# Performance work log

Hardware: AMD Instinct MI355X
Metric: run time of the kernel (lower is better)

Reference implementation:

```python
import jax, jax.numpy as jnp
import numpy as np

B, S, D, H, HZ = 4096, 64, 9, 128, 32
DT = 0.1


def _lstm_cell(x, h, c, Wih, Whh, bih, bhh):
    gates = x @ Wih.T + bih + h @ Whh.T + bhh
    i, f, g, o = jnp.split(gates, 4, axis=-1)
    c_new = jax.nn.sigmoid(f) * c + jax.nn.sigmoid(i) * jnp.tanh(g)
    h_new = jax.nn.sigmoid(o) * jnp.tanh(c_new)
    return h_new, c_new


def _forward(input_batch, W_ih_enc, W_hh_enc, b_ih_enc, b_hh_enc, W_e, V_e, v_e,
             W_d, V_d, v_d, W_ih_dec, W_hh_dec, b_ih_dec, b_hh_dec,
             W_out, b_out, scaler_mean, scaler_std, pos_mean):
    bsz = input_batch.shape[0]
    # ---- encoder with input attention ----
    x_perm = jnp.swapaxes(input_batch, 1, 2)          # (B, D, S)
    attn_input = jnp.einsum('bds,ts->bdt', x_perm, V_e)  # V_e * x^i, precomputed once
    h0 = jnp.zeros((bsz, H), input_batch.dtype)
    c0 = jnp.zeros((bsz, H), input_batch.dtype)

    def enc_step(carry, x_t):
        h, c = carry
        attn_hidden = jnp.concatenate([h, c], axis=1) @ W_e.T          # (B, S)
        comb = jnp.tanh(attn_hidden[:, None, :] + attn_input)          # (B, D, S)
        e = comb @ v_e                                                 # (B, D)
        alpha = jax.nn.softmax(e, axis=1)
        h, c = _lstm_cell(alpha * x_t, h, c, W_ih_enc, W_hh_enc, b_ih_enc, b_hh_enc)
        return (h, c), h

    (h_enc, c_enc), hs = jax.lax.scan(enc_step, (h0, c0), jnp.swapaxes(input_batch, 0, 1))
    enc_hidden = jnp.swapaxes(hs, 0, 1)               # (B, S, H)
    attn_encoder = enc_hidden @ V_d.T                 # V_d * h_j, precomputed once

    # ---- initial physics state ----
    pos = input_batch[:, -1, :3] + pos_mean
    vel = input_batch[:, -1, 3:6] * scaler_std + scaler_mean
    pre_vel = input_batch[:, -2, 3:6] * scaler_std + scaler_mean
    acc = (vel - pre_vel) / DT

    def dec_step(carry, _):
        d, c, pos, vel, acc = carry
        attn_dec = jnp.concatenate([d, c], axis=1) @ W_d.T             # (B, H)
        comb = jnp.tanh(attn_dec[:, None, :] + attn_encoder)           # (B, S, H)
        beta = jax.nn.softmax(comb @ v_d, axis=1)                      # (B, S)
        context = jnp.einsum('bs,bsh->bh', beta, enc_hidden)           # (B, H)
        phys = jnp.concatenate([pos - pos_mean,
                                (vel - scaler_mean) / scaler_std,
                                acc / scaler_std], axis=1)             # (B, 9)
        d, c = _lstm_cell(jnp.concatenate([phys, context], axis=1), d, c,
                          W_ih_dec, W_hh_dec, b_ih_dec, b_hh_dec)
        pred_acc = (jnp.concatenate([d, context], axis=1) @ W_out.T + b_out) * scaler_std
        pos_pred = pos + vel * DT + 0.5 * acc * DT * DT                # Verlet position
        vel_new = vel + 0.5 * (acc + pred_acc) * DT                    # Verlet velocity
        out = jnp.concatenate([pos_pred, vel_new, pred_acc], axis=1)   # (B, 9)
        return (d, c, pos_pred, vel_new, pred_acc), out

    _, outs = jax.lax.scan(dec_step, (h_enc, c_enc, pos, vel, acc), None, length=HZ)
    return jnp.swapaxes(outs, 0, 1)                   # (B, HZ, 9)


def setup_inputs() -> dict:
    key = jax.random.key(0)
    ks = jax.random.split(key, 16)
    p = lambda k, shape, s=0.05: jax.random.normal(k, shape, dtype=jnp.float32) * s
    return dict(
        input_batch=jax.random.normal(ks[0], (B, S, D), dtype=jnp.float32),
        W_ih_enc=p(ks[1], (4 * H, D)), W_hh_enc=p(ks[2], (4 * H, H)),
        b_ih_enc=jnp.zeros((4 * H,), jnp.float32), b_hh_enc=jnp.zeros((4 * H,), jnp.float32),
        W_e=p(ks[3], (S, 2 * H)), V_e=p(ks[4], (S, S)), v_e=p(ks[5], (S,)),
        W_d=p(ks[6], (H, 2 * H)), V_d=p(ks[7], (H, H)), v_d=p(ks[8], (H,)),
        W_ih_dec=p(ks[9], (4 * H, 9 + H)), W_hh_dec=p(ks[10], (4 * H, H)),
        b_ih_dec=jnp.zeros((4 * H,), jnp.float32), b_hh_dec=jnp.zeros((4 * H,), jnp.float32),
        W_out=p(ks[11], (3, 2 * H)), b_out=jnp.zeros((3,), jnp.float32),
        scaler_mean=p(ks[12], (3,), 0.1),
        scaler_std=jnp.abs(p(ks[13], (3,), 0.1)) + 1.0,
        pos_mean=p(ks[14], (3,), 0.1),
    )


def reference(input_batch, W_ih_enc, W_hh_enc, b_ih_enc, b_hh_enc, W_e, V_e, v_e,
              W_d, V_d, v_d, W_ih_dec, W_hh_dec, b_ih_dec, b_hh_dec,
              W_out, b_out, scaler_mean, scaler_std, pos_mean):
    return _forward(input_batch, W_ih_enc, W_hh_enc, b_ih_enc, b_hh_enc, W_e, V_e, v_e,
                    W_d, V_d, v_d, W_ih_dec, W_hh_dec, b_ih_dec, b_hh_dec,
                    W_out, b_out, scaler_mean, scaler_std, pos_mean)
```

## Files before the change

kernel.cpp:

```cpp
#include <hip/hip_runtime.h>
#include <hip/hip_bf16.h>
#include <hip/hip_fp8.h>

#define B_   4096
#define S_   64
#define D_   9
#define H_   128
#define HZ_  32
#define DT_  0.1f

#define OFF_WET    0
#define OFF_VET    16384
#define OFF_WENCT  20480
#define OFF_BENC   90624
#define OFF_WDT    91136
#define OFF_WDECT  123904
#define OFF_BDEC   259584
#define OFF_WOUTT  260096
#define OFF_VDT    260864
#define OFF_DECD   277248
#define OFF_DECC   801536
#define F32_TOTAL  1325824
#define PREP_N     277248


typedef __bf16 bf16x8 __attribute__((ext_vector_type(8)));
typedef float  f32x4  __attribute__((ext_vector_type(4)));

__device__ __forceinline__ float fast_tanh(float x) {
    float e = __expf(2.0f * x);
    return 1.0f - __fdividef(2.0f, e + 1.0f);
}
__device__ __forceinline__ float sigf(float x) {
    return __fdividef(1.0f, 1.0f + __expf(-x));
}
__device__ __forceinline__ float bf_lo(unsigned int u) { return __uint_as_float(u << 16); }
__device__ __forceinline__ float bf_hi(unsigned int u) { return __uint_as_float(u & 0xffff0000u); }
__device__ __forceinline__ float bfu2f(unsigned short u) { return __uint_as_float((unsigned int)u << 16); }
__device__ __forceinline__ unsigned short f2bfu(float f) {
    __hip_bfloat16 b = __float2bfloat16(f);
    return *(unsigned short*)&b;
}
__device__ __forceinline__ unsigned int pack_bf(float lo, float hi) {
    return (unsigned int)f2bfu(lo) | ((unsigned int)f2bfu(hi) << 16);
}
__device__ __forceinline__ float f8tof(unsigned int byte) {
    __hip_fp8_e4m3 t; t.__x = (unsigned char)byte; return (float)t;
}
__device__ __forceinline__ unsigned char f2f8(float f) {
    __hip_fp8_e4m3 q(f); return q.__x;
}
__device__ __forceinline__ unsigned int pack4_f8(float a, float b, float c, float d) {
    return (unsigned int)f2f8(a) | ((unsigned int)f2f8(b) << 8) |
           ((unsigned int)f2f8(c) << 16) | ((unsigned int)f2f8(d) << 24);
}

__global__ void prep_kernel(const float* __restrict__ Wih_e, const float* __restrict__ Whh_e,
    const float* __restrict__ bih_e, const float* __restrict__ bhh_e,
    const float* __restrict__ W_e, const float* __restrict__ V_e,
    const float* __restrict__ W_d, const float* __restrict__ V_d,
    const float* __restrict__ Wih_d, const float* __restrict__ Whh_d,
    const float* __restrict__ bih_d, const float* __restrict__ bhh_d,
    const float* __restrict__ W_out, float* __restrict__ ws) {
  for (int idx = blockIdx.x * blockDim.x + threadIdx.x; idx < PREP_N;
       idx += gridDim.x * blockDim.x) {
    int i = idx;
    if (i < 16384) { continue; }
    i -= 16384;
    if (i < 4096) { int s = i >> 6, t = i & 63; ws[OFF_VET + i] = V_e[t * 64 + s]; continue; }
    i -= 4096;
    if (i < 70144) { continue; }
    i -= 70144;
    if (i < 512) { ws[OFF_BENC + i] = bih_e[i] + bhh_e[i]; continue; }
    i -= 512;
    if (i < 32768) { continue; }
    i -= 32768;
    if (i < 135680) { continue; }
    i -= 135680;
    if (i < 512) { ws[OFF_BDEC + i] = bih_d[i] + bhh_d[i]; continue; }
    i -= 512;
    if (i < 768) { int k = i / 3, j = i % 3; ws[OFF_WOUTT + i] = W_out[j * 256 + k]; continue; }
  }
}

__global__ void prep_mfma_kernel(const float* __restrict__ W_d,
    const float* __restrict__ Wih_d, const float* __restrict__ Whh_d,
    unsigned short* __restrict__ WdTm, unsigned short* __restrict__ WdecTm) {
  int idx = blockIdx.x * blockDim.x + threadIdx.x;
  if (idx < 32768) {
    int j = idx & 7, l = (idx >> 3) & 63, t = idx >> 9;
    int nt = t & 7, ks = t >> 3;
    int k = ks * 32 + (l >> 4) * 8 + j;
    int n = nt * 16 + (l & 15);
    WdTm[idx] = f2bfu(W_d[n * 256 + k]);
    return;
  }
  int i2 = idx - 32768;
  if (i2 < 147456) {
    int j = i2 & 7, l = (i2 >> 3) & 63, t = i2 >> 9;
    int ks = t % 9, tile = t / 9;
    int q = tile & 3, is = tile >> 2;
    int k = ks * 32 + (l >> 4) * 8 + j;
    int g = q * 128 + is * 16 + (l & 15);
    float v;
    if (k < 128)      v = Whh_d[g * 128 + k];
    else if (k < 256) v = Wih_d[g * 137 + 9 + (k - 128)];
    else if (k < 265) v = Wih_d[g * 137 + (k - 256)];
    else              v = 0.f;
    WdecTm[i2] = f2bfu(v);
  }
}

__global__ void prep_enc_mfma_kernel(const float* __restrict__ W_e,
    const float* __restrict__ Wih_e, const float* __restrict__ Whh_e,
    const float* __restrict__ V_d,
    unsigned short* __restrict__ WeTm, unsigned short* __restrict__ WencTm,
    unsigned short* __restrict__ VdTm) {
  int idx = blockIdx.x * blockDim.x + threadIdx.x;
  if (idx < 16384) {
    int j = idx & 7, l = (idx >> 3) & 63, tile = idx >> 9;
    int nt = tile & 3, ks = tile >> 2;
    int k = ks * 32 + (l >> 4) * 8 + j;
    int n = nt * 16 + (l & 15);
    WeTm[idx] = f2bfu(W_e[n * 256 + k]);
    return;
  }
  int i2 = idx - 16384;
  if (i2 < 81920) {
    int j = i2 & 7, l = (i2 >> 3) & 63, tile = i2 >> 9;
    int ks = tile % 5, tq = tile / 5;
    int q = tq & 3, is = tq >> 2;
    int kk = (l >> 4) * 8 + j;
    int g = q * 128 + is * 16 + (l & 15);
    float v;
    if (ks < 4) v = Whh_e[g * 128 + ks * 32 + kk];
    else        v = (kk < 9) ? Wih_e[g * 9 + kk] : 0.f;
    WencTm[i2] = f2bfu(v);
    return;
  }
  int i3 = i2 - 81920;
  if (i3 < 16384) {
    int j = i3 & 7, l = (i3 >> 3) & 63, tile = i3 >> 9;
    int nt = tile & 7, ks = tile >> 3;
    int i = ks * 32 + (l >> 4) * 8 + j;
    int n = nt * 16 + (l & 15);
    VdTm[i3] = f2bfu(V_d[n * 128 + i]);
  }
}

__global__ __launch_bounds__(512, 1) void encoder_mfma_kernel(
    const float* __restrict__ x_in, const float* __restrict__ ws,
    const float* __restrict__ v_e_g,
    const unsigned short* __restrict__ WeTm, const unsigned short* __restrict__ WencTm,
    __hip_bfloat16* __restrict__ EH,
    unsigned short* __restrict__ dG, float* __restrict__ cG) {
  __shared__ unsigned short hA[2][16 * 296];
  __shared__ float cF[16 * 132];
  __shared__ float ahL[16 * 64];
  __shared__ unsigned short aiL[16 * 576];
  __shared__ unsigned short xbL[16 * 576];

  const int tid = threadIdx.x;
  const int b0 = blockIdx.x * 16;
  const int l = tid & 63, w = tid >> 6;
  const int quad = l >> 4, l15 = l & 15;

  for (int i = tid; i < 16 * 576; i += 512) {
    int m = i / 576, r = i % 576;
    xbL[i] = f2bfu(x_in[(size_t)(b0 + m) * 576 + r]);
  }
  for (int i = tid; i < 2 * 16 * 296; i += 512) ((unsigned short*)hA)[i] = 0;
  for (int i = tid; i < 16 * 132; i += 512) cF[i] = 0.f;
  __syncthreads();

  {
    const float* __restrict__ VeT = ws + OFF_VET;
    for (int i = tid; i < 16 * 576; i += 512) {
      int t = i & 63, dd = (i >> 6) % 9, m = i / 576;
      float acc = 0.f;
      for (int s = 0; s < 64; ++s) acc += bfu2f(xbL[m * 576 + s * 9 + dd]) * VeT[s * 64 + t];
      aiL[m * 576 + dd * 64 + t] = f2bfu(acc);
    }
  }
  const float ve_r = v_e_g[l];
  const int ig = w * 16 + l15;
  float bbq[4];
  #pragma unroll
  for (int q = 0; q < 4; ++q) bbq[q] = ws[OFF_BENC + q * 128 + ig];
  __syncthreads();

  for (int t = 0; t < S_; ++t) {
    unsigned short* bufC = hA[t & 1];
    unsigned short* bufN = hA[(t + 1) & 1];
    if (w < 4) {
      f32x4 acc = {0.f, 0.f, 0.f, 0.f};
      #pragma unroll
      for (int ks = 0; ks < 8; ++ks) {
        uint4 au = *(const uint4*)&bufC[l15 * 296 + ks * 32 + quad * 8];
        uint4 bu = *(const uint4*)(WeTm + (size_t)((ks * 4 + w) * 64 + l) * 8);
        acc = __builtin_amdgcn_mfma_f32_16x16x32_bf16(
            __builtin_bit_cast(bf16x8, au), __builtin_bit_cast(bf16x8, bu), acc, 0, 0, 0);
      }
      #pragma unroll
      for (int r = 0; r < 4; ++r)
        ahL[(quad * 4 + r) * 64 + w * 16 + l15] = acc[r];
    }
    __syncthreads();
    {
      const int m0 = 2 * w, m1 = 2 * w + 1;
      float a0 = ahL[m0 * 64 + l], a1 = ahL[m1 * 64 + l];
      float e0k = -1e30f, e1k = -1e30f;
      #pragma unroll
      for (int dd = 0; dd < 9; ++dd) {
        float t0 = fast_tanh(a0 + bfu2f(aiL[m0 * 576 + dd * 64 + l])) * ve_r;
        float t1 = fast_tanh(a1 + bfu2f(aiL[m1 * 576 + dd * 64 + l])) * ve_r;
        #pragma unroll
        for (int off = 32; off; off >>= 1) {
          t0 += __shfl_xor(t0, off, 64);
          t1 += __shfl_xor(t1, off, 64);
        }
        if (l == dd) { e0k = t0; e1k = t1; }
      }
      float mx0 = e0k, mx1 = e1k;
      #pragma unroll
      for (int off = 8; off; off >>= 1) {
        mx0 = fmaxf(mx0, __shfl_xor(mx0, off, 64));
        mx1 = fmaxf(mx1, __shfl_xor(mx1, off, 64));
      }
      float ex0 = (l < 9) ? __expf(e0k - mx0) : 0.f;
      float ex1 = (l < 9) ? __expf(e1k - mx1) : 0.f;
      float s0 = ex0, s1 = ex1;
      #pragma unroll
      for (int off = 8; off; off >>= 1) {
        s0 += __shfl_xor(s0, off, 64);
        s1 += __shfl_xor(s1, off, 64);
      }
      if (l < 9) {
        bufC[m0 * 296 + 256 + l] = f2bfu(__fdividef(ex0, s0) * bfu2f(xbL[m0 * 576 + t * 9 + l]));
        bufC[m1 * 296 + 256 + l] = f2bfu(__fdividef(ex1, s1) * bfu2f(xbL[m1 * 576 + t * 9 + l]));
      }
    }
    __syncthreads();
    {
      uint4 af[5];
      #pragma unroll
      for (int ks = 0; ks < 4; ++ks)
        af[ks] = *(const uint4*)&bufC[l15 * 296 + ks * 32 + quad * 8];
      af[4] = *(const uint4*)&bufC[l15 * 296 + 256 + quad * 8];
      f32x4 g4[4];
      #pragma unroll
      for (int q = 0; q < 4; ++q) {
        f32x4 acc = {0.f, 0.f, 0.f, 0.f};
        #pragma unroll
        for (int ks = 0; ks < 5; ++ks) {
          uint4 bu = *(const uint4*)(WencTm + (size_t)(((w * 4 + q) * 5 + ks) * 64 + l) * 8);
          acc = __builtin_amdgcn_mfma_f32_16x16x32_bf16(
              __builtin_bit_cast(bf16x8, af[ks]), __builtin_bit_cast(bf16x8, bu), acc, 0, 0, 0);
        }
        g4[q] = acc;
      }
      #pragma unroll
      for (int r = 0; r < 4; ++r) {
        int m = quad * 4 + r;
        float gi = g4[0][r] + bbq[0];
        float gf = g4[1][r] + bbq[1];
        float gg = g4[2][r] + bbq[2];
        float go = g4[3][r] + bbq[3];
        float co = cF[m * 132 + ig];
        float cn = sigf(gf) * co + sigf(gi) * fast_tanh(gg);
        float hn = sigf(go) * fast_tanh(cn);
        cF[m * 132 + ig] = cn;
        bufN[m * 296 + ig] = f2bfu(hn);
        bufN[m * 296 + 128 + ig] = f2bfu(cn);
        EH[((size_t)(b0 + m) * S_ + t) * H_ + ig] = __float2bfloat16(hn);
      }
    }
    __syncthreads();
  }
  for (int i = tid; i < 16 * 128; i += 512) {
    int m = i >> 7, ii = i & 127;
    dG[(size_t)(b0 + m) * 128 + ii] = hA[0][m * 296 + ii];
    cG[(size_t)(b0 + m) * 128 + ii] = cF[m * 132 + ii];
  }
}

__global__ __launch_bounds__(256) void attnenc_mfma_kernel(
    const unsigned short* __restrict__ EH, const unsigned short* __restrict__ VdTm,
    unsigned char* __restrict__ AETf8, unsigned char* __restrict__ EHf8) {
  const int tid = threadIdx.x;
  const int b = blockIdx.x * 4 + (tid >> 6);
  const int l = tid & 63;
  const int quad = l >> 4, l15 = l & 15;

  const unsigned short* ehb = EH + (size_t)b * 8192;
  uint4 A[4][4];
  #pragma unroll
  for (int st = 0; st < 4; ++st)
    #pragma unroll
    for (int ks = 0; ks < 4; ++ks)
      A[st][ks] = *(const uint4*)(ehb + (st * 16 + l15) * 128 + ks * 32 + quad * 8);

  {
    unsigned char* e8b = EHf8 + (size_t)b * 8192;
    #pragma unroll
    for (int st = 0; st < 4; ++st)
      #pragma unroll
      for (int ks = 0; ks < 4; ++ks) {
        uint4 a = A[st][ks];
        uint2 pk;
        pk.x = pack4_f8(bf_lo(a.x), bf_hi(a.x), bf_lo(a.y), bf_hi(a.y));
        pk.y = pack4_f8(bf_lo(a.z), bf_hi(a.z), bf_lo(a.w), bf_hi(a.w));
        *(uint2*)(e8b + (st * 16 + l15) * 128 + ks * 32 + quad * 8) = pk;
      }
  }

  unsigned char* outb = AETf8 + (size_t)b * 8192;
  const int k = l15;
  #pragma unroll
  for (int nt = 0; nt < 8; ++nt) {
    uint4 Bf[4];
    #pragma unroll
    for (int ks = 0; ks < 4; ++ks)
      Bf[ks] = *(const uint4*)(VdTm + (size_t)((ks * 8 + nt) * 64 + l) * 8);
    int kg = nt * 16 + k;
    int kb = kg >> 3, k7 = kg & 7;
    #pragma unroll
    for (int st = 0; st < 4; ++st) {
      f32x4 acc = {0.f, 0.f, 0.f, 0.f};
      #pragma unroll
      for (int ks = 0; ks < 4; ++ks)
        acc = __builtin_amdgcn_mfma_f32_16x16x32_bf16(
            __builtin_bit_cast(bf16x8, A[st][ks]), __builtin_bit_cast(bf16x8, Bf[ks]), acc, 0, 0, 0);
      #pragma unroll
      for (int r = 0; r < 4; ++r) {
        int s = st * 16 + quad * 4 + r;
        outb[kb * 512 + s * 8 + k7] = f2f8(acc[r]);
      }
    }
  }
}

__global__ __launch_bounds__(256) void init_dec_kernel(
    const float* __restrict__ x_in,
    const unsigned short* __restrict__ dG, const float* __restrict__ cG,
    const unsigned short* __restrict__ WdTm,
    const float* __restrict__ smean_g, const float* __restrict__ sstd_g,
    const float* __restrict__ pmean_g,
    unsigned short* __restrict__ adG, float* __restrict__ pvsG) {
  __shared__ unsigned short dcB[16 * 264];
  const int tid = threadIdx.x;
  const int b0 = blockIdx.x * 16;
  const int l = tid & 63, w = tid >> 6;
  const int quad = l >> 4, l15 = l & 15;

  {
    int m = tid >> 4, i0 = (tid & 15) * 8;
    *(uint4*)&dcB[m * 264 + i0] = *(const uint4*)(dG + (size_t)(b0 + m) * 128 + i0);
    float4 c0 = *(const float4*)(cG + (size_t)(b0 + m) * 128 + i0);
    float4 c1 = *(const float4*)(cG + (size_t)(b0 + m) * 128 + i0 + 4);
    uint4 pk;
    pk.x = pack_bf(c0.x, c0.y); pk.y = pack_bf(c0.z, c0.w);
    pk.z = pack_bf(c1.x, c1.y); pk.w = pack_bf(c1.z, c1.w);
    *(uint4*)&dcB[m * 264 + 128 + i0] = pk;
  }
  if (tid < 48) {
    int m = tid / 3, jj = tid % 3;
    const float* xi = x_in + (size_t)(b0 + m) * 576;
    float sm = smean_g[jj], ss = sstd_g[jj], pm = pmean_g[jj];
    float v  = xi[63 * 9 + 3 + jj] * ss + sm;
    float pv = xi[62 * 9 + 3 + jj] * ss + sm;
    float* P = pvsG + (size_t)(b0 + m) * 12;
    P[jj] = xi[63 * 9 + jj] + pm;
    P[3 + jj] = v;
    P[6 + jj] = (v - pv) / DT_;
  }
  __syncthreads();
  #pragma unroll
  for (int t = 0; t < 2; ++t) {
    const int nt = w + 4 * t;
    f32x4 acc = {0.f, 0.f, 0.f, 0.f};
    #pragma unroll
    for (int ks = 0; ks < 8; ++ks) {
      uint4 au = *(const uint4*)&dcB[l15 * 264 + ks * 32 + quad * 8];
      uint4 bu = *(const uint4*)(WdTm + (size_t)((ks * 8 + nt) * 64 + l) * 8);
      acc = __builtin_amdgcn_mfma_f32_16x16x32_bf16(
          __builtin_bit_cast(bf16x8, au), __builtin_bit_cast(bf16x8, bu), acc, 0, 0, 0);
    }
    int n = nt * 16 + l15;
    #pragma unroll
    for (int r = 0; r < 4; ++r)
      adG[(size_t)(b0 + quad * 4 + r) * 128 + n] = f2bfu(acc[r]);
  }
}

__global__ __launch_bounds__(256, 8) void attn_step_kernel(
    const unsigned char* __restrict__ AETf8, const unsigned char* __restrict__ EHf8,
    const unsigned short* __restrict__ adG, const float* __restrict__ v_d_g,
    unsigned short* __restrict__ ctxG) {
  __shared__ unsigned short adL[2 * 128];
  __shared__ float vdL[128];
  __shared__ float scp[2][2][64];
  __shared__ float bet[2][64];
  __shared__ float ctxP[2][2][128];

  const int tid = threadIdx.x;
  const int b0 = blockIdx.x * 2;
  const int l = tid & 63, w = tid >> 6;
  const int ml = w >> 1, half = w & 1;
  const int quad = l >> 4, l15 = l & 15;

  if (tid < 32)
    *(uint4*)&adL[tid * 8] = *(const uint4*)(adG + (size_t)(b0 + (tid >> 4)) * 128 + (tid & 15) * 8);
  if (tid < 128) vdL[tid] = v_d_g[tid];
  __syncthreads();

  {
    const unsigned char* aet = AETf8 + (size_t)(b0 + ml) * 8192 + (size_t)half * 8 * 512;
    const unsigned short* adp = adL + ml * 128 + half * 64;
    float e = 0.f;
    #pragma unroll
    for (int kb = 0; kb < 8; ++kb) {
      uint2 av = *(const uint2*)(aet + kb * 512 + l * 8);
      uint4 ad8 = *(const uint4*)(adp + kb * 8);
      float4 v0 = *(const float4*)&vdL[half * 64 + kb * 8];
      float4 v1 = *(const float4*)&vdL[half * 64 + kb * 8 + 4];
      e += fast_tanh(bf_lo(ad8.x) + f8tof(av.x))       * v0.x;
      e += fast_tanh(bf_hi(ad8.x) + f8tof(av.x >> 8))  * v0.y;
      e += fast_tanh(bf_lo(ad8.y) + f8tof(av.x >> 16)) * v0.z;
      e += fast_tanh(bf_hi(ad8.y) + f8tof(av.x >> 24)) * v0.w;
      e += fast_tanh(bf_lo(ad8.z) + f8tof(av.y))       * v1.x;
      e += fast_tanh(bf_hi(ad8.z) + f8tof(av.y >> 8))  * v1.y;
      e += fast_tanh(bf_lo(ad8.w) + f8tof(av.y >> 16)) * v1.z;
      e += fast_tanh(bf_hi(ad8.w) + f8tof(av.y >> 24)) * v1.w;
    }
    scp[ml][half][l] = e;
  }
  __syncthreads();
  if (half == 0) {
    float e = scp[ml][0][l] + scp[ml][1][l];
    float mx = e;
    #pragma unroll
    for (int off = 32; off; off >>= 1) mx = fmaxf(mx, __shfl_xor(mx, off, 64));
    float ex = __expf(e - mx);
    float ss = ex;
    #pragma unroll
    for (int off = 32; off; off >>= 1) ss += __shfl_xor(ss, off, 64);
    bet[ml][l] = __fdividef(ex, ss);
  }
  __syncthreads();
  {
    const unsigned char* base = EHf8 + (size_t)(b0 + ml) * 8192 + (size_t)half * 32 * 128;
    float a[8];
    #pragma unroll
    for (int r = 0; r < 8; ++r) a[r] = 0.f;
    #pragma unroll
    for (int it = 0; it < 8; ++it) {
      int sl = it * 4 + quad;
      uint2 ev = *(const uint2*)(base + sl * 128 + l15 * 8);
      float bt = bet[ml][half * 32 + sl];
      a[0] += bt * f8tof(ev.x);       a[1] += bt * f8tof(ev.x >> 8);
      a[2] += bt * f8tof(ev.x >> 16); a[3] += bt * f8tof(ev.x >> 24);
      a[4] += bt * f8tof(ev.y);       a[5] += bt * f8tof(ev.y >> 8);
      a[6] += bt * f8tof(ev.y >> 16); a[7] += bt * f8tof(ev.y >> 24);
    }
    #pragma unroll
    for (int r = 0; r < 8; ++r) {
      a[r] += __shfl_xor(a[r], 16, 64);
      a[r] += __shfl_xor(a[r], 32, 64);
    }
    if (quad == 0) {
      *(float4*)&ctxP[ml][half][l15 * 8]     = make_float4(a[0], a[1], a[2], a[3]);
      *(float4*)&ctxP[ml][half][l15 * 8 + 4] = make_float4(a[4], a[5], a[6], a[7]);
    }
  }
  __syncthreads();
  if (tid < 128) {
    int mi = tid >> 6, hp = (tid & 63) * 2;
    float c0 = ctxP[mi][0][hp]     + ctxP[mi][1][hp];
    float c1 = ctxP[mi][0][hp + 1] + ctxP[mi][1][hp + 1];
    *(unsigned int*)(ctxG + (size_t)(b0 + mi) * 128 + hp) = pack_bf(c0, c1);
  }
}

__global__ __launch_bounds__(512, 2) void gemm_step_kernel(
    const float* __restrict__ ws,
    const unsigned short* __restrict__ dG_in, float* __restrict__ cG,
    const unsigned short* __restrict__ ctxG,
    const unsigned short* __restrict__ WdTm, const unsigned short* __restrict__ WdecTm,
    unsigned short* __restrict__ dG_out, unsigned short* __restrict__ adG,
    float* __restrict__ pvsG,
    const float* __restrict__ b_out_g, const float* __restrict__ smean_g,
    const float* __restrict__ sstd_g, const float* __restrict__ pmean_g,
    float* __restrict__ out, int hz) {
  __shared__ unsigned short gA[16 * 296];
  __shared__ unsigned short dcB[16 * 264];
  __shared__ float pd[16 * 3 * 8];
  __shared__ float pc[16 * 3 * 4];

  const int tid = threadIdx.x;
  const int b0 = blockIdx.x * 16;
  const int l = tid & 63, w = tid >> 6;
  const int quad = l >> 4, l15 = l & 15;

  if (tid < 256) {
    int m = tid >> 4, i0 = (tid & 15) * 8;
    *(uint4*)&gA[m * 296 + i0] = *(const uint4*)(dG_in + (size_t)(b0 + m) * 128 + i0);
  } else {
    int t = tid - 256;
    int m = t >> 4, i0 = (t & 15) * 8;
    *(uint4*)&gA[m * 296 + 128 + i0] = *(const uint4*)(ctxG + (size_t)(b0 + m) * 128 + i0);
  }
  if (tid < 496) { int mm = tid / 31, r = tid % 31; gA[mm * 296 + 265 + r] = 0; }
  if (tid < 48) {
    int m = tid / 3, jj = tid % 3;
    const float* P = pvsG + (size_t)(b0 + m) * 12;
    float sm = smean_g[jj], ss = sstd_g[jj], pm = pmean_g[jj];
    gA[m * 296 + 256 + jj]     = f2bfu(P[jj] - pm);
    gA[m * 296 + 256 + 3 + jj] = f2bfu((P[3 + jj] - sm) / ss);
    gA[m * 296 + 256 + 6 + jj] = f2bfu(P[6 + jj] / ss);
  }
  __syncthreads();

  {
    uint4 af[9];
    #pragma unroll
    for (int ks = 0; ks < 9; ++ks)
      af[ks] = *(const uint4*)&gA[l15 * 296 + ks * 32 + quad * 8];
    const int is = w, i = is * 16 + l15;
    float bb[4], wd[3];
    #pragma unroll
    for (int q = 0; q < 4; ++q) bb[q] = ws[OFF_BDEC + q * 128 + i];
    #pragma unroll
    for (int jj = 0; jj < 3; ++jj) wd[jj] = ws[OFF_WOUTT + i * 3 + jj];
    f32x4 g4[4];
    #pragma unroll
    for (int q = 0; q < 4; ++q) {
      f32x4 acc = {0.f, 0.f, 0.f, 0.f};
      #pragma unroll
      for (int ks = 0; ks < 9; ++ks) {
        uint4 bu = *(const uint4*)(WdecTm + (size_t)(((is * 4 + q) * 9 + ks) * 64 + l) * 8);
        acc = __builtin_amdgcn_mfma_f32_16x16x32_bf16(
            __builtin_bit_cast(bf16x8, af[ks]), __builtin_bit_cast(bf16x8, bu), acc, 0, 0, 0);
      }
      g4[q] = acc;
    }
    float pr[4][3];
    #pragma unroll
    for (int r = 0; r < 4; ++r) {
      int m = quad * 4 + r;
      float gi = g4[0][r] + bb[0];
      float gf = g4[1][r] + bb[1];
      float gg = g4[2][r] + bb[2];
      float go = g4[3][r] + bb[3];
      float co = cG[(size_t)(b0 + m) * 128 + i];
      float cn = sigf(gf) * co + sigf(gi) * fast_tanh(gg);
      float hn = sigf(go) * fast_tanh(cn);
      cG[(size_t)(b0 + m) * 128 + i] = cn;
      unsigned short hb = f2bfu(hn);
      dG_out[(size_t)(b0 + m) * 128 + i] = hb;
      dcB[m * 264 + i] = hb;
      dcB[m * 264 + 128 + i] = f2bfu(cn);
      pr[r][0] = hn * wd[0]; pr[r][1] = hn * wd[1]; pr[r][2] = hn * wd[2];
    }
    #pragma unroll
    for (int r = 0; r < 4; ++r)
      #pragma unroll
      for (int jj = 0; jj < 3; ++jj) {
        float v = pr[r][jj];
        #pragma unroll
        for (int off = 8; off; off >>= 1) v += __shfl_xor(v, off, 64);
        pr[r][jj] = v;
      }
    if (l15 == 0) {
      #pragma unroll
      for (int r = 0; r < 4; ++r)
        #pragma unroll
        for (int jj = 0; jj < 3; ++jj)
          pd[((quad * 4 + r) * 3 + jj) * 8 + is] = pr[r][jj];
    }
  }
  __syncthreads();

  {
    const int nt = w;
    f32x4 acc = {0.f, 0.f, 0.f, 0.f};
    #pragma unroll
    for (int ks = 0; ks < 8; ++ks) {
      uint4 au = *(const uint4*)&dcB[l15 * 264 + ks * 32 + quad * 8];
      uint4 bu = *(const uint4*)(WdTm + (size_t)((ks * 8 + nt) * 64 + l) * 8);
      acc = __builtin_amdgcn_mfma_f32_16x16x32_bf16(
          __builtin_bit_cast(bf16x8, au), __builtin_bit_cast(bf16x8, bu), acc, 0, 0, 0);
    }
    int n = nt * 16 + l15;
    #pragma unroll
    for (int r = 0; r < 4; ++r) {
      int m = quad * 4 + r;
      adG[(size_t)(b0 + m) * 128 + n] = f2bfu(acc[r]);
    }
  }
  if (tid < 192) {
    int m = tid / 12, jj = (tid % 12) / 4, part = tid % 4;
    int k0 = part * 32;
    float acc = 0.f;
    for (int k = k0; k < k0 + 32; ++k) {
      __hip_bfloat16 hv = *(__hip_bfloat16*)&gA[m * 296 + 128 + k];
      acc += __bfloat162float(hv) * ws[OFF_WOUTT + 384 + k * 3 + jj];
    }
    pc[(m * 3 + jj) * 4 + part] = acc;
  }
  __syncthreads();

  if (tid < 48) {
    int m = tid / 3, jj = tid % 3;
    float s = b_out_g[jj];
    #pragma unroll
    for (int p = 0; p < 4; ++p) s += pc[(m * 3 + jj) * 4 + p];
    #pragma unroll
    for (int is = 0; is < 8; ++is) s += pd[(m * 3 + jj) * 8 + is];
    float pacc = s * sstd_g[jj];
    float* P = pvsG + (size_t)(b0 + m) * 12;
    float pos = P[jj], vel = P[3 + jj], acc = P[6 + jj];
    float ppred = pos + vel * DT_ + 0.5f * acc * DT_ * DT_;
    float vnew  = vel + 0.5f * (acc + pacc) * DT_;
    size_t ob = ((size_t)(b0 + m) * HZ_ + hz) * 9;
    out[ob + jj] = ppred; out[ob + 3 + jj] = vnew; out[ob + 6 + jj] = pacc;
    P[jj] = ppred; P[3 + jj] = vnew; P[6 + jj] = pacc;
  }
}

extern "C" void kernel_launch(void* const* d_in, const int* in_sizes, int n_in,
                              void* d_out, int out_size, void* d_ws, size_t ws_size,
                              hipStream_t stream) {
  (void)in_sizes; (void)n_in; (void)out_size; (void)ws_size;
  const float* x      = (const float*)d_in[0];
  const float* Wih_e  = (const float*)d_in[1];
  const float* Whh_e  = (const float*)d_in[2];
  const float* bih_e  = (const float*)d_in[3];
  const float* bhh_e  = (const float*)d_in[4];
  const float* W_e    = (const float*)d_in[5];
  const float* V_e    = (const float*)d_in[6];
  const float* v_e    = (const float*)d_in[7];
  const float* W_d    = (const float*)d_in[8];
  const float* V_d    = (const float*)d_in[9];
  const float* v_d    = (const float*)d_in[10];
  const float* Wih_d  = (const float*)d_in[11];
  const float* Whh_d  = (const float*)d_in[12];
  const float* bih_d  = (const float*)d_in[13];
  const float* bhh_d  = (const float*)d_in[14];
  const float* W_out  = (const float*)d_in[15];
  const float* b_out  = (const float*)d_in[16];
  const float* smean  = (const float*)d_in[17];
  const float* sstd   = (const float*)d_in[18];
  const float* pmean  = (const float*)d_in[19];

  float* ws = (float*)d_ws;
  float* pvsG = ws;
  unsigned short* WeTm   = (unsigned short*)(ws + OFF_WET);
  unsigned short* WencTm = (unsigned short*)(ws + OFF_WENCT);
  unsigned short* WdTm   = (unsigned short*)(ws + OFF_WDT);
  unsigned short* WdecTm = (unsigned short*)(ws + OFF_WDECT);
  unsigned short* VdTm   = (unsigned short*)(ws + OFF_VDT);
  unsigned short* dG     = (unsigned short*)(ws + OFF_DECD);
  unsigned short* ctxG   = dG + 524288;
  float* cG = ws + OFF_DECC;
  unsigned short* ub  = (unsigned short*)(ws + F32_TOTAL);
  unsigned short* EH  = ub;
  unsigned char*  AETf8 = (unsigned char*)(ub + 33554432);
  unsigned char*  EHf8  = AETf8 + (size_t)B_ * 8192;
  unsigned short* adG = ub + 67108864;
  float* out = (float*)d_out;

  prep_kernel<<<(PREP_N + 255) / 256, 256, 0, stream>>>(
      Wih_e, Whh_e, bih_e, bhh_e, W_e, V_e, W_d, V_d,
      Wih_d, Whh_d, bih_d, bhh_d, W_out, ws);
  prep_mfma_kernel<<<(32768 + 147456 + 255) / 256, 256, 0, stream>>>(
      W_d, Wih_d, Whh_d, WdTm, WdecTm);
  prep_enc_mfma_kernel<<<(16384 + 81920 + 16384 + 255) / 256, 256, 0, stream>>>(
      W_e, Wih_e, Whh_e, V_d, WeTm, WencTm, VdTm);
  encoder_mfma_kernel<<<B_ / 16, 512, 0, stream>>>(
      x, ws, v_e, WeTm, WencTm, (__hip_bfloat16*)EH, dG, cG);
  attnenc_mfma_kernel<<<B_ / 4, 256, 0, stream>>>(EH, VdTm, AETf8, EHf8);
  init_dec_kernel<<<B_ / 16, 256, 0, stream>>>(
      x, dG, cG, WdTm, smean, sstd, pmean, adG, pvsG);
  for (int hz = 0; hz < HZ_; ++hz) {
    attn_step_kernel<<<B_ / 2, 256, 0, stream>>>(AETf8, EHf8, adG, v_d, ctxG);
    gemm_step_kernel<<<B_ / 16, 512, 0, stream>>>(
        ws, dG, cG, ctxG, WdTm, WdecTm, dG, adG, pvsG,
        b_out, smean, sstd, pmean, out, hz);
  }
}
```

Baseline: 1.693 ms.

## Fuse decoder attention step into the gemm step kernel

Measured after the change: 1.938 ms. +14.5%, slower.

```diff
diff --git a/kernel.cpp b/kernel.cpp
--- a/kernel.cpp
+++ b/kernel.cpp
@@ -393,37 +393,61 @@
   }
 }
 
-__global__ __launch_bounds__(256, 8) void attn_step_kernel(
+__global__ __launch_bounds__(512, 2) void dec_step_kernel(
+    const float* __restrict__ ws,
     const unsigned char* __restrict__ AETf8, const unsigned char* __restrict__ EHf8,
-    const unsigned short* __restrict__ adG, const float* __restrict__ v_d_g,
-    unsigned short* __restrict__ ctxG) {
-  __shared__ unsigned short adL[2 * 128];
+    const unsigned short* __restrict__ dG_in, float* __restrict__ cG,
+    const unsigned short* __restrict__ WdTm, const unsigned short* __restrict__ WdecTm,
+    unsigned short* __restrict__ dG_out, unsigned short* __restrict__ adG,
+    float* __restrict__ pvsG, const float* __restrict__ v_d_g,
+    const float* __restrict__ b_out_g, const float* __restrict__ smean_g,
+    const float* __restrict__ sstd_g, const float* __restrict__ pmean_g,
+    float* __restrict__ out, int hz) {
+  __shared__ unsigned short adL[16 * 128];
   __shared__ float vdL[128];
-  __shared__ float scp[2][2][64];
-  __shared__ float bet[2][64];
-  __shared__ float ctxP[2][2][128];
+  __shared__ float bet[16 * 64];
+  __shared__ unsigned short gA[16 * 296];
+  __shared__ unsigned short dcB[16 * 264];
+  __shared__ float pd[16 * 3 * 8];
+  __shared__ float pc[16 * 3 * 4];
 
   const int tid = threadIdx.x;
-  const int b0 = blockIdx.x * 2;
+  const int b0 = blockIdx.x * 16;
   const int l = tid & 63, w = tid >> 6;
-  const int ml = w >> 1, half = w & 1;
   const int quad = l >> 4, l15 = l & 15;
 
-  if (tid < 32)
-    *(uint4*)&adL[tid * 8] = *(const uint4*)(adG + (size_t)(b0 + (tid >> 4)) * 128 + (tid & 15) * 8);
+  if (tid < 256) {
+    int m = tid >> 4, i0 = (tid & 15) * 8;
+    *(uint4*)&gA[m * 296 + i0] = *(const uint4*)(dG_in + (size_t)(b0 + m) * 128 + i0);
+  } else {
+    int t = tid - 256;
+    int m = t >> 4, i0 = (t & 15) * 8;
+    *(uint4*)&adL[m * 128 + i0] = *(const uint4*)(adG + (size_t)(b0 + m) * 128 + i0);
+  }
   if (tid < 128) vdL[tid] = v_d_g[tid];
+  if (tid < 496) { int mm = tid / 31, r = tid % 31; gA[mm * 296 + 265 + r] = 0; }
+  if (tid < 48) {
+    int m = tid / 3, jj = tid % 3;
+    const float* P = pvsG + (size_t)(b0 + m) * 12;
+    float sm = smean_g[jj], ss = sstd_g[jj], pm = pmean_g[jj];
+    gA[m * 296 + 256 + jj]     = f2bfu(P[jj] - pm);
+    gA[m * 296 + 256 + 3 + jj] = f2bfu((P[3 + jj] - sm) / ss);
+    gA[m * 296 + 256 + 6 + jj] = f2bfu(P[6 + jj] / ss);
+  }
   __syncthreads();
 
-  {
-    const unsigned char* aet = AETf8 + (size_t)(b0 + ml) * 8192 + (size_t)half * 8 * 512;
-    const unsigned short* adp = adL + ml * 128 + half * 64;
+  #pragma unroll
+  for (int u = 0; u < 2; ++u) {
+    const int mi = 2 * w + u;
+    const unsigned char* aet = AETf8 + (size_t)(b0 + mi) * 8192;
+    const unsigned short* adp = adL + mi * 128;
     float e = 0.f;
     #pragma unroll
-    for (int kb = 0; kb < 8; ++kb) {
+    for (int kb = 0; kb < 16; ++kb) {
       uint2 av = *(const uint2*)(aet + kb * 512 + l * 8);
       uint4 ad8 = *(const uint4*)(adp + kb * 8);
-      float4 v0 = *(const float4*)&vdL[half * 64 + kb * 8];
-      float4 v1 = *(const float4*)&vdL[half * 64 + kb * 8 + 4];
+      float4 v0 = *(const float4*)&vdL[kb * 8];
+      float4 v1 = *(const float4*)&vdL[kb * 8 + 4];
       e += fast_tanh(bf_lo(ad8.x) + f8tof(av.x))       * v0.x;
       e += fast_tanh(bf_hi(ad8.x) + f8tof(av.x >> 8))  * v0.y;
       e += fast_tanh(bf_lo(ad8.y) + f8tof(av.x >> 16)) * v0.z;
@@ -433,31 +457,24 @@
       e += fast_tanh(bf_lo(ad8.w) + f8tof(av.y >> 16)) * v1.z;
       e += fast_tanh(bf_hi(ad8.w) + f8tof(av.y >> 24)) * v1.w;
     }
-    scp[ml][half][l] = e;
-  }
-  __syncthreads();
-  if (half == 0) {
-    float e = scp[ml][0][l] + scp[ml][1][l];
-    float mx = e;
-    #pragma unroll
-    for (int off = 32; off; off >>= 1) mx = fmaxf(mx, __shfl_xor(mx, off, 64));
-    float ex = __expf(e - mx);
+    float ex = __expf(e);
     float ss = ex;
     #pragma unroll
     for (int off = 32; off; off >>= 1) ss += __shfl_xor(ss, off, 64);
-    bet[ml][l] = __fdividef(ex, ss);
-  }
-  __syncthreads();
-  {
-    const unsigned char* base = EHf8 + (size_t)(b0 + ml) * 8192 + (size_t)half * 32 * 128;
+    bet[mi * 64 + l] = __fdividef(ex, ss);
+  }
+  #pragma unroll
+  for (int u = 0; u < 2; ++u) {
+    const int mi = 2 * w + u;
+    const unsigned char* base = EHf8 + (size_t)(b0 + mi) * 8192;
     float a[8];
     #pragma unroll
     for (int r = 0; r < 8; ++r) a[r] = 0.f;
     #pragma unroll
-    for (int it = 0; it < 8; ++it) {
+    for (int it = 0; it < 16; ++it) {
       int sl = it * 4 + quad;
       uint2 ev = *(const uint2*)(base + sl * 128 + l15 * 8);
-      float bt = bet[ml][half * 32 + sl];
+      float bt = bet[mi * 64 + sl];
       a[0] += bt * f8tof(ev.x);       a[1] += bt * f8tof(ev.x >> 8);
       a[2] += bt * f8tof(ev.x >> 16); a[3] += bt * f8tof(ev.x >> 24);
       a[4] += bt * f8tof(ev.y);       a[5] += bt * f8tof(ev.y >> 8);
@@ -469,55 +486,11 @@
       a[r] += __shfl_xor(a[r], 32, 64);
     }
     if (quad == 0) {
-      *(float4*)&ctxP[ml][half][l15 * 8]     = make_float4(a[0], a[1], a[2], a[3]);
-      *(float4*)&ctxP[ml][half][l15 * 8 + 4] = make_float4(a[4], a[5], a[6], a[7]);
-    }
-  }
-  __syncthreads();
-  if (tid < 128) {
-    int mi = tid >> 6, hp = (tid & 63) * 2;
-    float c0 = ctxP[mi][0][hp]     + ctxP[mi][1][hp];
-    float c1 = ctxP[mi][0][hp + 1] + ctxP[mi][1][hp + 1];
-    *(unsigned int*)(ctxG + (size_t)(b0 + mi) * 128 + hp) = pack_bf(c0, c1);
-  }
-}
-
-__global__ __launch_bounds__(512, 2) void gemm_step_kernel(
-    const float* __restrict__ ws,
-    const unsigned short* __restrict__ dG_in, float* __restrict__ cG,
-    const unsigned short* __restrict__ ctxG,
-    const unsigned short* __restrict__ WdTm, const unsigned short* __restrict__ WdecTm,
-    unsigned short* __restrict__ dG_out, unsigned short* __restrict__ adG,
-    float* __restrict__ pvsG,
-    const float* __restrict__ b_out_g, const float* __restrict__ smean_g,
-    const float* __restrict__ sstd_g, const float* __restrict__ pmean_g,
-    float* __restrict__ out, int hz) {
-  __shared__ unsigned short gA[16 * 296];
-  __shared__ unsigned short dcB[16 * 264];
-  __shared__ float pd[16 * 3 * 8];
-  __shared__ float pc[16 * 3 * 4];
-
-  const int tid = threadIdx.x;
-  const int b0 = blockIdx.x * 16;
-  const int l = tid & 63, w = tid >> 6;
-  const int quad = l >> 4, l15 = l & 15;
-
-  if (tid < 256) {
-    int m = tid >> 4, i0 = (tid & 15) * 8;
-    *(uint4*)&gA[m * 296 + i0] = *(const uint4*)(dG_in + (size_t)(b0 + m) * 128 + i0);
-  } else {
-    int t = tid - 256;
-    int m = t >> 4, i0 = (t & 15) * 8;
-    *(uint4*)&gA[m * 296 + 128 + i0] = *(const uint4*)(ctxG + (size_t)(b0 + m) * 128 + i0);
-  }
-  if (tid < 496) { int mm = tid / 31, r = tid % 31; gA[mm * 296 + 265 + r] = 0; }
-  if (tid < 48) {
-    int m = tid / 3, jj = tid % 3;
-    const float* P = pvsG + (size_t)(b0 + m) * 12;
-    float sm = smean_g[jj], ss = sstd_g[jj], pm = pmean_g[jj];
-    gA[m * 296 + 256 + jj]     = f2bfu(P[jj] - pm);
-    gA[m * 296 + 256 + 3 + jj] = f2bfu((P[3 + jj] - sm) / ss);
-    gA[m * 296 + 256 + 6 + jj] = f2bfu(P[6 + jj] / ss);
+      uint4 pk;
+      pk.x = pack_bf(a[0], a[1]); pk.y = pack_bf(a[2], a[3]);
+      pk.z = pack_bf(a[4], a[5]); pk.w = pack_bf(a[6], a[7]);
+      *(uint4*)&gA[mi * 296 + 128 + l15 * 8] = pk;
+    }
   }
   __syncthreads();
 
@@ -661,7 +634,6 @@
   unsigned short* WdecTm = (unsigned short*)(ws + OFF_WDECT);
   unsigned short* VdTm   = (unsigned short*)(ws + OFF_VDT);
   unsigned short* dG     = (unsigned short*)(ws + OFF_DECD);
-  unsigned short* ctxG   = dG + 524288;
   float* cG = ws + OFF_DECC;
   unsigned short* ub  = (unsigned short*)(ws + F32_TOTAL);
   unsigned short* EH  = ub;
@@ -683,9 +655,8 @@
   init_dec_kernel<<<B_ / 16, 256, 0, stream>>>(
       x, dG, cG, WdTm, smean, sstd, pmean, adG, pvsG);
   for (int hz = 0; hz < HZ_; ++hz) {
-    attn_step_kernel<<<B_ / 2, 256, 0, stream>>>(AETf8, EHf8, adG, v_d, ctxG);
-    gemm_step_kernel<<<B_ / 16, 512, 0, stream>>>(
-        ws, dG, cG, ctxG, WdTm, WdecTm, dG, adG, pvsG,
-        b_out, smean, sstd, pmean, out, hz);
-  }
-}
+    dec_step_kernel<<<B_ / 16, 512, 0, stream>>>(
+        ws, AETf8, EHf8, dG, cG, WdTm, WdecTm, dG, adG, pvsG,
+        v_d, b_out, smean, sstd, pmean, out, hz);
+  }
+}
```
